# Kernel tuning notes

Hardware: AMD Instinct MI355X
Metric: run time of the kernel (lower is better)

## Reference

```python
import jax, jax.numpy as jnp
import numpy as np

N = 1_000_000          # number of RoIs
C = 4                  # num_class (foreground classes)
IMG_H, IMG_W = 1080.0, 1920.0
BBOX_MEAN = jnp.array([0.0, 0.0, 0.0, 0.0], jnp.float32)
BBOX_STD = jnp.array([0.1, 0.1, 0.2, 0.2], jnp.float32)
THR_OBJ = 0.2          # threshold_objectness
THR_CLS = 0.1          # thresholds[0]
MIN_W, MIN_H = 6.0, 6.0
MAX_CAND = 300         # nms max_candidate_n
OVERLAP = 0.5          # nms overlap_ratio
TOP_N = 100            # nms top_n


def setup_inputs() -> dict:
    key = jax.random.key(0)
    k1, k2, k3, k4, k5 = jax.random.split(key, 5)
    logits = jax.random.normal(k1, (N, C + 1), jnp.float32) * 2.0
    cls_score_softmax = jax.nn.softmax(logits, axis=-1)          # rows sum to 1, like softmax output
    bbox_pred = jax.random.normal(k2, (N, 4 * (C + 1)), jnp.float32) * 0.5
    x1 = jax.random.uniform(k3, (N,), jnp.float32, 0.0, IMG_W * 0.8)
    y1 = jax.random.uniform(k4, (N,), jnp.float32, 0.0, IMG_H * 0.8)
    wh = jax.random.uniform(k5, (N, 2), jnp.float32, 8.0, 200.0)
    rois = jnp.stack([jnp.zeros((N,), jnp.float32), x1, y1, x1 + wh[:, 0], y1 + wh[:, 1]], axis=1)
    im_info = jnp.array([IMG_H, IMG_W], jnp.float32)
    return {"cls_score_softmax": cls_score_softmax, "bbox_pred": bbox_pred, "rois": rois, "im_info": im_info}


def _pairwise_iou(b):
    # torchvision box_iou convention: area = (x2-x1)*(y2-y1), no +1
    lt = jnp.maximum(b[:, None, :2], b[None, :, :2])
    rb = jnp.minimum(b[:, None, 2:], b[None, :, 2:])
    wh = jnp.clip(rb - lt, 0.0)
    inter = wh[..., 0] * wh[..., 1]
    area = (b[:, 2] - b[:, 0]) * (b[:, 3] - b[:, 1])
    return inter / (area[:, None] + area[None, :] - inter)


def _forward(cls_score_softmax, bbox_pred, rois, im_info):
    h_img, w_img = im_info[0], im_info[1]
    # denormalize deltas and decode against rois (bbox_transform_inv_rcnn)
    deltas = (bbox_pred.reshape(-1, 4) * BBOX_STD + BBOX_MEAN).reshape(-1, C + 1, 4)
    bx = rois[:, 1:]
    w = bx[:, 2] - bx[:, 0] + 1.0
    h = bx[:, 3] - bx[:, 1] + 1.0
    cx = bx[:, 0] + 0.5 * (w - 1.0)
    cy = bx[:, 1] + 0.5 * (h - 1.0)
    pcx = deltas[:, :, 0] * w[:, None] + cx[:, None]
    pcy = deltas[:, :, 1] * h[:, None] + cy[:, None]
    pw = jnp.exp(deltas[:, :, 2]) * w[:, None]
    ph = jnp.exp(deltas[:, :, 3]) * h[:, None]
    pred = jnp.stack([pcx - 0.5 * (pw - 1.0), pcy - 0.5 * (ph - 1.0),
                      pcx + 0.5 * (pw - 1.0), pcy + 0.5 * (ph - 1.0)], axis=-1)  # [N, C+1, 4]
    # refine_out_of_map_bbox: clip to image
    pred = jnp.stack([jnp.clip(pred[..., 0], 0.0, w_img - 1.0),
                      jnp.clip(pred[..., 1], 0.0, h_img - 1.0),
                      jnp.clip(pred[..., 2], 0.0, w_img - 1.0),
                      jnp.clip(pred[..., 3], 0.0, h_img - 1.0)], axis=-1)
    # objectness + class-score filters (masked instead of compacted: jit-friendly)
    mask_obj = (1.0 - cls_score_softmax[:, 0]) >= THR_OBJ
    maxes = jnp.max(cls_score_softmax[:, 1:], axis=1)
    argmaxes = jnp.argmax(cls_score_softmax[:, 1:], axis=1) + 1
    mask_cls = maxes > THR_CLS
    # select the box of the argmax class per row
    box = jnp.take_along_axis(pred, argmaxes[:, None, None], axis=1)[:, 0, :]  # [N, 4]
    bw = box[:, 2] - box[:, 0] + 1.0
    bh = box[:, 3] - box[:, 1] + 1.0
    mask_size = (bw >= MIN_W) | (bh >= MIN_H)  # HEIGHT_OR_WIDTH
    valid = mask_obj & mask_cls & mask_size
    # top-k candidates by max class prob (invalid rows pushed below any real score)
    cand_scores = jnp.where(valid, maxes, -1.0)
    top_vals, top_idx = jax.lax.top_k(cand_scores, MAX_CAND)   # sorted descending
    cand_boxes = box[top_idx]                                   # [M, 4]
    cand_probs = cls_score_softmax[top_idx]                     # [M, C+1]
    cand_valid = top_vals > -0.5
    # greedy NMS over the (score-sorted) candidates
    iou = _pairwise_iou(cand_boxes)
    idx = jnp.arange(MAX_CAND)

    def body(i, keep):
        sup = keep[i] & (iou[i] > OVERLAP) & (idx > i)
        return keep & ~sup

    keep = jax.lax.fori_loop(0, MAX_CAND, body, cand_valid)
    # compact kept rows into the first TOP_N slots (drop-row scatter trick)
    order = jnp.cumsum(keep.astype(jnp.int32)) - 1
    slot = jnp.where(keep & (order < TOP_N), order, TOP_N)
    rows = jnp.concatenate([jnp.zeros((MAX_CAND, 1), cand_boxes.dtype), cand_boxes, cand_probs], axis=1)
    out = jnp.zeros((TOP_N + 1, rows.shape[1]), rows.dtype).at[slot].set(rows)[:TOP_N]
    return out  # [TOP_N, 1 + 4 + (C+1)] = [100, 10], zero-padded past the kept count


def reference(cls_score_softmax, bbox_pred, rois, im_info):
    return _forward(cls_score_softmax, bbox_pred, rois, im_info)
```

## Files before the change

### kernel.cpp

```cpp
#include <hip/hip_runtime.h>
#include <math.h>

#define NBINS 4096
#define CAP   4096
#define MAXC  300
#define MAXCP 320
#define TOPN  100

__device__ __forceinline__ int bin_of(float s) {
    int b = (int)(s * (float)NBINS);
    return b > NBINS-1 ? NBINS-1 : b;
}
__device__ __forceinline__ int subbin_of(float s, int tau) {
    float f = s * (float)NBINS - (float)tau;
    int sb = (int)(f * (float)NBINS);
    sb = sb < 0 ? 0 : (sb > NBINS-1 ? NBINS-1 : sb);
    return sb;
}

__device__ __forceinline__ unsigned long long rdlane64(unsigned long long v, int lane) {
    unsigned int lo = (unsigned int)__builtin_amdgcn_readlane((int)(unsigned int)(v & 0xFFFFFFFFull), lane);
    unsigned int hi = (unsigned int)__builtin_amdgcn_readlane((int)(unsigned int)(v >> 32), lane);
    return ((unsigned long long)hi << 32) | (unsigned long long)lo;
}

__device__ __forceinline__ void decode4(float x1, float y1, float x2, float y2,
                                        float4 d4, float Wimg, float Himg,
                                        float& bx1, float& by1, float& bx2, float& by2)
{
    float w  = x2 - x1 + 1.0f;
    float h  = y2 - y1 + 1.0f;
    float cx = x1 + 0.5f*(w - 1.0f);
    float cy = y1 + 0.5f*(h - 1.0f);
    float d0 = d4.x*0.1f, d1 = d4.y*0.1f, d2 = d4.z*0.2f, d3 = d4.w*0.2f;
    float pcx = d0*w + cx;
    float pcy = d1*h + cy;
    float pw  = expf(d2)*w;
    float ph  = expf(d3)*h;
    bx1 = fminf(fmaxf(pcx - 0.5f*(pw-1.0f), 0.0f), Wimg-1.0f);
    by1 = fminf(fmaxf(pcy - 0.5f*(ph-1.0f), 0.0f), Himg-1.0f);
    bx2 = fminf(fmaxf(pcx + 0.5f*(pw-1.0f), 0.0f), Wimg-1.0f);
    by2 = fminf(fmaxf(pcy + 0.5f*(ph-1.0f), 0.0f), Himg-1.0f);
}

__global__ __launch_bounds__(256)
void rcnn_pass1(const float4* __restrict__ cls4, const float4* __restrict__ bbox4,
                const float4* __restrict__ rois4, const float* __restrict__ iminfo,
                float4* __restrict__ scores4,
                unsigned int* __restrict__ hist, unsigned int* __restrict__ hist2,
                unsigned int* __restrict__ counter, int Ng)
{
    if (blockIdx.x == 0) {
        for (int k = threadIdx.x; k < NBINS; k += 256) { hist[k] = 0u; hist2[k] = 0u; }
        if (threadIdx.x == 0) *counter = 0u;
    }

    int g = blockIdx.x * blockDim.x + threadIdx.x;
    if (g >= Ng) return;

    float c[20], q[20];
    #pragma unroll
    for (int v = 0; v < 5; v++) {
        float4 cv = cls4[5*g + v];
        c[4*v] = cv.x; c[4*v+1] = cv.y; c[4*v+2] = cv.z; c[4*v+3] = cv.w;
        float4 rv = rois4[5*g + v];
        q[4*v] = rv.x; q[4*v+1] = rv.y; q[4*v+2] = rv.z; q[4*v+3] = rv.w;
    }
    float Himg = iminfo[0], Wimg = iminfo[1];

    float s[4];
    #pragma unroll
    for (int j = 0; j < 4; j++) {
        float p0 = c[5*j], p1 = c[5*j+1], p2 = c[5*j+2], p3 = c[5*j+3], p4 = c[5*j+4];
        float m = p1; int a = 1;
        if (p2 > m) { m = p2; a = 2; }
        if (p3 > m) { m = p3; a = 3; }
        if (p4 > m) { m = p4; a = 4; }
        float sc = -1.0f;
        if (((1.0f - p0) >= 0.2f) && (m > 0.1f)) {
            float4 d4 = bbox4[20*g + 5*j + a];
            float bx1, by1, bx2, by2;
            decode4(q[5*j+1], q[5*j+2], q[5*j+3], q[5*j+4], d4, Wimg, Himg, bx1, by1, bx2, by2);
            float bw = bx2 - bx1 + 1.0f;
            float bh = by2 - by1 + 1.0f;
            if ((bw >= 6.0f) || (bh >= 6.0f)) sc = m;
        }
        s[j] = sc;
    }
    scores4[g] = make_float4(s[0], s[1], s[2], s[3]);
}

__global__ __launch_bounds__(1024)
void rcnn_hist(const float4* __restrict__ scores4, unsigned int* __restrict__ hist, int Ng)
{
    __shared__ unsigned int lh[NBINS];
    const int t = threadIdx.x;
    for (int k = t; k < NBINS; k += 1024) lh[k] = 0u;
    __syncthreads();
    int stride = gridDim.x * 1024;
    for (int g = blockIdx.x * 1024 + t; g < Ng; g += stride) {
        float4 s4 = scores4[g];
        float ss[4] = { s4.x, s4.y, s4.z, s4.w };
        #pragma unroll
        for (int j = 0; j < 4; j++)
            if (ss[j] > -0.5f) atomicAdd(&lh[bin_of(ss[j])], 1u);
    }
    __syncthreads();
    for (int k = t; k < NBINS; k += 1024) {
        unsigned int v = lh[k];
        if (v) atomicAdd(&hist[k], v);
    }
}

__global__ __launch_bounds__(1024)
void rcnn_pass2(const unsigned int* __restrict__ hist, int* __restrict__ taubin)
{
    __shared__ unsigned int suf[1024];
    __shared__ int g_sh;
    int t = threadIdx.x;
    suf[t] = hist[4*t] + hist[4*t+1] + hist[4*t+2] + hist[4*t+3];
    __syncthreads();
    for (int d = 1; d < 1024; d <<= 1) {
        unsigned int add = (t + d < 1024) ? suf[t + d] : 0u;
        __syncthreads();
        suf[t] += add;
        __syncthreads();
    }
    if (t == 0) g_sh = -1;
    __syncthreads();
    if (suf[t] >= MAXC && (t == 1023 || suf[t+1] < MAXC)) g_sh = t;
    __syncthreads();
    if (t == 0) {
        int g = g_sh;
        int tau = 0;
        if (g >= 0) {
            unsigned int cum = (g == 1023) ? 0u : suf[g+1];
            tau = 4*g;
            for (int k = 3; k >= 0; k--) {
                cum += hist[4*g + k];
                if (cum >= MAXC) { tau = 4*g + k; break; }
            }
        }
        *taubin = tau;
    }
}

__global__ __launch_bounds__(1024)
void rcnn_hist2(const float4* __restrict__ scores4, const int* __restrict__ taubin,
                unsigned int* __restrict__ hist2, int Ng)
{
    __shared__ unsigned int lh[NBINS];
    const int t = threadIdx.x;
    const int tau = *taubin;
    for (int k = t; k < NBINS; k += 1024) lh[k] = 0u;
    __syncthreads();
    int stride = gridDim.x * 1024;
    for (int g = blockIdx.x * 1024 + t; g < Ng; g += stride) {
        float4 s4 = scores4[g];
        float ss[4] = { s4.x, s4.y, s4.z, s4.w };
        #pragma unroll
        for (int j = 0; j < 4; j++)
            if (ss[j] > -0.5f && bin_of(ss[j]) == tau)
                atomicAdd(&lh[subbin_of(ss[j], tau)], 1u);
    }
    __syncthreads();
    for (int k = t; k < NBINS; k += 1024) {
        unsigned int v = lh[k];
        if (v) atomicAdd(&hist2[k], v);
    }
}

__global__ __launch_bounds__(1024)
void rcnn_pass2b(const unsigned int* __restrict__ hist, const unsigned int* __restrict__ hist2,
                 const int* __restrict__ taubin, int* __restrict__ tau2out)
{
    __shared__ unsigned int red[1024];
    __shared__ unsigned int suf[1024];
    __shared__ int g_sh;
    __shared__ unsigned int need_sh;
    int t = threadIdx.x;
    int tau = *taubin;
    unsigned int acc = 0;
    for (int k = tau + 1 + t; k < NBINS; k += 1024) acc += hist[k];
    red[t] = acc;
    __syncthreads();
    for (int d = 512; d > 0; d >>= 1) { if (t < d) red[t] += red[t + d]; __syncthreads(); }
    if (t == 0) {
        unsigned int C1 = red[0];
        need_sh = (C1 >= MAXC) ? 1u : (unsigned int)(MAXC - C1);
    }
    __syncthreads();
    unsigned int need = need_sh;
    suf[t] = hist2[4*t] + hist2[4*t+1] + hist2[4*t+2] + hist2[4*t+3];
    __syncthreads();
    for (int d = 1; d < 1024; d <<= 1) {
        unsigned int add = (t + d < 1024) ? suf[t + d] : 0u;
        __syncthreads();
        suf[t] += add;
        __syncthreads();
    }
    if (t == 0) g_sh = -1;
    __syncthreads();
    if (suf[t] >= need && (t == 1023 || suf[t+1] < need)) g_sh = t;
    __syncthreads();
    if (t == 0) {
        int g = g_sh;
        int tau2 = 0;
        if (g >= 0) {
            unsigned int cum = (g == 1023) ? 0u : suf[g+1];
            tau2 = 4*g;
            for (int k = 3; k >= 0; k--) {
                cum += hist2[4*g + k];
                if (cum >= need) { tau2 = 4*g + k; break; }
            }
        }
        *tau2out = tau2;
    }
}

__global__ __launch_bounds__(256)
void rcnn_pass3(const float4* __restrict__ scores4, const int* __restrict__ taubin,
                const int* __restrict__ tau2bin,
                unsigned long long* __restrict__ ckey,
                unsigned int* __restrict__ counter, int Ng)
{
    int g = blockIdx.x * blockDim.x + threadIdx.x;
    if (g >= Ng) return;
    float4 s4 = scores4[g];
    int tau = *taubin, tau2 = *tau2bin;
    float ss[4] = { s4.x, s4.y, s4.z, s4.w };
    #pragma unroll
    for (int j = 0; j < 4; j++) {
        float s = ss[j];
        if (s > -0.5f) {
            int bin = bin_of(s);
            bool sel = (bin > tau) || (bin == tau && subbin_of(s, tau) >= tau2);
            if (sel) {
                unsigned int pos = atomicAdd(counter, 1u);
                if (pos < CAP) {
                    unsigned int idx = (unsigned int)(4*g + j);
                    ckey[pos] = ((unsigned long long)__float_as_uint(s) << 32)
                              | (unsigned long long)(~idx);
                }
            }
        }
    }
}

__global__ __launch_bounds__(1024)
void rcnn_prep(const float* __restrict__ cls, const float* __restrict__ bbox,
               const float* __restrict__ rois, const float* __restrict__ iminfo,
               const unsigned long long* __restrict__ ckey,
               const unsigned int* __restrict__ counter,
               unsigned long long* __restrict__ sup_g,
               float4* __restrict__ bx4_g,
               float* __restrict__ pr_g,
               unsigned long long* __restrict__ maskw_g)
{
    __shared__ unsigned long long skey[CAP];
    __shared__ int    tid_[MAXC];
    __shared__ float4 bx4[MAXCP];
    __shared__ unsigned long long maskw[5];
    const int t  = threadIdx.x;
    const int NT = 1024;
    int M = (int)*counter; if (M > CAP) M = CAP;

    for (int i = t; i < M; i += NT)  skey[i] = ckey[i];
    for (int r = t; r < MAXC; r += NT) tid_[r] = -1;
    for (int r = t; r < MAXCP; r += NT) bx4[r] = make_float4(0.f, 0.f, 0.f, 0.f);
    if (t < 5) maskw[t] = 0ull;
    __syncthreads();

    for (int i = t; i < M; i += NT) {
        unsigned long long ki = skey[i];
        int r = 0;
        for (int j = 0; j < M; j++) r += (skey[j] > ki);
        if (r < MAXC) tid_[r] = (int)(~(unsigned int)ki);
    }
    __syncthreads();

    float Himg = iminfo[0], Wimg = iminfo[1];
    for (int r = t; r < MAXC; r += NT) {
        int i = tid_[r];
        if (i >= 0) {
            pr_g[5*r+0] = cls[5*i];   pr_g[5*r+1] = cls[5*i+1];
            pr_g[5*r+2] = cls[5*i+2]; pr_g[5*r+3] = cls[5*i+3];
            pr_g[5*r+4] = cls[5*i+4];
            float p1 = cls[5*i+1], p2 = cls[5*i+2], p3 = cls[5*i+3], p4 = cls[5*i+4];
            float m = p1; int a = 1;
            if (p2 > m) { m = p2; a = 2; }
            if (p3 > m) { m = p3; a = 3; }
            if (p4 > m) { m = p4; a = 4; }
            float4 d4 = ((const float4*)bbox)[5*i + a];
            float bx1, by1, bx2, by2;
            decode4(rois[5*i+1], rois[5*i+2], rois[5*i+3], rois[5*i+4], d4, Wimg, Himg, bx1, by1, bx2, by2);
            float4 B = make_float4(bx1, by1, bx2, by2);
            bx4[r] = B;
            bx4_g[r] = B;
            atomicOr(&maskw[r>>6], 1ull << (r & 63));
        }
    }
    __syncthreads();

    if (t < 5) maskw_g[t] = maskw[t];

    for (int task = t; task < MAXC*5; task += NT) {
        int w = task / MAXC;
        int i = task - w*MAXC;
        unsigned long long bits = 0ull;
        int j0 = w << 6;
        if (j0 + 63 > i) {
            float4 A = bx4[i];
            float areaA = (A.z - A.x)*(A.w - A.y);
            for (int b = 0; b < 64; b++) {
                float4 B = bx4[j0 + b];
                float lx = fmaxf(A.x, B.x), ly = fmaxf(A.y, B.y);
                float rx = fminf(A.z, B.z), ry = fminf(A.w, B.w);
                float iw = fmaxf(rx - lx, 0.0f), ih = fmaxf(ry - ly, 0.0f);
                float inter = iw * ih;
                float areaB = (B.z - B.x)*(B.w - B.y);
                float iou = inter / (areaA + areaB - inter);
                bits |= (iou > 0.5f) ? (1ull << b) : 0ull;
            }
            unsigned long long jgt = (i < j0) ? ~0ull
                                  : ((i - j0) >= 63 ? 0ull : ~((1ull << (i - j0 + 1)) - 1ull));
            bits &= jgt & maskw[w];
        }
        sup_g[i*5 + w] = bits;
    }
}

__global__ __launch_bounds__(64, 1)
void rcnn_nms(const unsigned long long* __restrict__ sup_g,
              const float4* __restrict__ bx4_g,
              const float* __restrict__ pr_g,
              const unsigned long long* __restrict__ maskw_g,
              float* __restrict__ out)
{
    __shared__ float orows[TOPN*10];
    const int l = threadIdx.x;

    unsigned long long A0 = sup_g[l*5+0], A1 = sup_g[l*5+1], A2 = sup_g[l*5+2],
                       A3 = sup_g[l*5+3], A4 = sup_g[l*5+4];
    unsigned long long B0 = sup_g[(64+l)*5+0], B1 = sup_g[(64+l)*5+1], B2 = sup_g[(64+l)*5+2],
                       B3 = sup_g[(64+l)*5+3], B4 = sup_g[(64+l)*5+4];
    unsigned long long C0 = sup_g[(128+l)*5+0], C1 = sup_g[(128+l)*5+1], C2 = sup_g[(128+l)*5+2],
                       C3 = sup_g[(128+l)*5+3], C4 = sup_g[(128+l)*5+4];
    unsigned long long D0 = sup_g[(192+l)*5+0], D1 = sup_g[(192+l)*5+1], D2 = sup_g[(192+l)*5+2],
                       D3 = sup_g[(192+l)*5+3], D4 = sup_g[(192+l)*5+4];
    bool e = (l < MAXC - 256);
    unsigned long long E0 = e ? sup_g[(256+l)*5+0] : 0ull,
                       E1 = e ? sup_g[(256+l)*5+1] : 0ull,
                       E2 = e ? sup_g[(256+l)*5+2] : 0ull,
                       E3 = e ? sup_g[(256+l)*5+3] : 0ull,
                       E4 = e ? sup_g[(256+l)*5+4] : 0ull;

    unsigned long long kw0 = maskw_g[0], kw1 = maskw_g[1], kw2 = maskw_g[2],
                       kw3 = maskw_g[3], kw4 = maskw_g[4];

#define SCAN_BLK(W0, W1, W2, W3, W4, KWREF, COUNT)                          \
    for (int s2 = 0; s2 < (COUNT); s2++) {                                  \
        unsigned long long m = ((KWREF >> s2) & 1ull) ? ~0ull : 0ull;       \
        kw0 &= ~(rdlane64(W0, s2) & m);                                     \
        kw1 &= ~(rdlane64(W1, s2) & m);                                     \
        kw2 &= ~(rdlane64(W2, s2) & m);                                     \
        kw3 &= ~(rdlane64(W3, s2) & m);                                     \
        kw4 &= ~(rdlane64(W4, s2) & m);                                     \
    }
    SCAN_BLK(A0, A1, A2, A3, A4, kw0, 64)
    SCAN_BLK(B0, B1, B2, B3, B4, kw1, 64)
    SCAN_BLK(C0, C1, C2, C3, C4, kw2, 64)
    SCAN_BLK(D0, D1, D2, D3, D4, kw3, 64)
    SCAN_BLK(E0, E1, E2, E3, E4, kw4, MAXC - 256)
#undef SCAN_BLK

    for (int k = l; k < TOPN*10; k += 64) orows[k] = 0.0f;
    __syncthreads();

    int p0 = __popcll(kw0), p1 = __popcll(kw1), p2 = __popcll(kw2), p3 = __popcll(kw3);
    unsigned long long lmask = (l == 0) ? 0ull : ((~0ull) >> (64 - l));

#define EMIT_BLK(KW, BASE, PRE)                                             \
    if ((KW >> l) & 1ull) {                                                 \
        int r   = (BASE) + l;                                               \
        int ord = (PRE) + __popcll(KW & lmask);                             \
        if (ord < TOPN) {                                                   \
            float4 B = bx4_g[r];                                            \
            float* row = &orows[ord*10];                                    \
            row[0] = 0.0f;                                                  \
            row[1] = B.x; row[2] = B.y; row[3] = B.z; row[4] = B.w;         \
            row[5] = pr_g[5*r+0]; row[6] = pr_g[5*r+1];                     \
            row[7] = pr_g[5*r+2]; row[8] = pr_g[5*r+3];                     \
            row[9] = pr_g[5*r+4];                                           \
        }                                                                   \
    }
    EMIT_BLK(kw0,   0, 0)
    EMIT_BLK(kw1,  64, p0)
    EMIT_BLK(kw2, 128, p0 + p1)
    EMIT_BLK(kw3, 192, p0 + p1 + p2)
    if (l < MAXC - 256) { EMIT_BLK(kw4, 256, p0 + p1 + p2 + p3) }
#undef EMIT_BLK
    __syncthreads();
    for (int k = l; k < TOPN*10; k += 64) out[k] = orows[k];
}

extern "C" void kernel_launch(void* const* d_in, const int* in_sizes, int n_in,
                              void* d_out, int out_size, void* d_ws, size_t ws_size,
                              hipStream_t stream)
{
    const float* cls    = (const float*)d_in[0];
    const float* bbox   = (const float*)d_in[1];
    const float* rois   = (const float*)d_in[2];
    const float* iminfo = (const float*)d_in[3];
    int N  = in_sizes[0] / 5;
    int Ng = N / 4;

    char* ws = (char*)d_ws;
    float* scores = (float*)ws;
    size_t off = ((size_t)N * 4 + 255) & ~(size_t)255;
    unsigned int* hist    = (unsigned int*)(ws + off); off += NBINS * 4;
    unsigned int* hist2   = (unsigned int*)(ws + off); off += NBINS * 4;
    int*          taubin  = (int*)(ws + off);          off += 256;
    int*          tau2bin = (int*)(ws + off);          off += 256;
    unsigned int* counter = (unsigned int*)(ws + off); off += 256;
    unsigned long long* ckey   = (unsigned long long*)(ws + off); off += CAP * 8;
    unsigned long long* sup_g  = (unsigned long long*)(ws + off); off += MAXC * 5 * 8 + 64;
    float4*             bx4_g  = (float4*)(ws + off);             off += MAXC * 16 + 64;
    float*              pr_g   = (float*)(ws + off);              off += MAXC * 5 * 4 + 64;
    unsigned long long* maskw_g= (unsigned long long*)(ws + off); off += 64;

    int blocksG = (Ng + 255) / 256;
    rcnn_pass1<<<blocksG, 256, 0, stream>>>((const float4*)cls, (const float4*)bbox,
                                            (const float4*)rois, iminfo,
                                            (float4*)scores, hist, hist2, counter, Ng);
    rcnn_hist<<<64, 1024, 0, stream>>>((const float4*)scores, hist, Ng);
    rcnn_pass2<<<1, 1024, 0, stream>>>(hist, taubin);
    rcnn_hist2<<<64, 1024, 0, stream>>>((const float4*)scores, taubin, hist2, Ng);
    rcnn_pass2b<<<1, 1024, 0, stream>>>(hist, hist2, taubin, tau2bin);
    rcnn_pass3<<<blocksG, 256, 0, stream>>>((const float4*)scores, taubin, tau2bin,
                                            ckey, counter, Ng);
    rcnn_prep<<<1, 1024, 0, stream>>>(cls, bbox, rois, iminfo, ckey, counter,
                                      sup_g, bx4_g, pr_g, maskw_g);
    rcnn_nms<<<1, 64, 0, stream>>>(sup_g, bx4_g, pr_g, maskw_g, (float*)d_out);
}
```

Before: 229.2 us.

## Fuse scoring with histogram and replace two-level threshold with single fine histogram

Scoring now builds a per-block LDS histogram in the same kernel, which removes a separate pass over the scores. The two-level 4096-bin histogram and its sub-bin refinement give way to a single 16384-bin histogram. Per-block partial histograms are reduced with no global atomics, and the last-arriving block computes the threshold bin, which cuts the launch count from eight to five. The prep kernel's IoU mask build now uses wave ballots instead of per-thread 64-iteration loops. In exchange, the coarser threshold may admit more candidates into compaction and the O(M²) rank sort, and a candidate count above CAP could truncate results.

```diff
diff --git a/kernel.cpp b/kernel.cpp
--- a/kernel.cpp
+++ b/kernel.cpp
@@ -1,21 +1,16 @@
 #include <hip/hip_runtime.h>
 #include <math.h>
 
-#define NBINS 4096
+#define NB1   16384
+#define NPART 256
 #define CAP   4096
 #define MAXC  300
 #define MAXCP 320
 #define TOPN  100
 
-__device__ __forceinline__ int bin_of(float s) {
-    int b = (int)(s * (float)NBINS);
-    return b > NBINS-1 ? NBINS-1 : b;
-}
-__device__ __forceinline__ int subbin_of(float s, int tau) {
-    float f = s * (float)NBINS - (float)tau;
-    int sb = (int)(f * (float)NBINS);
-    sb = sb < 0 ? 0 : (sb > NBINS-1 ? NBINS-1 : sb);
-    return sb;
+__device__ __forceinline__ int bin16(float s) {
+    int b = (int)(s * (float)NB1);
+    return b > NB1-1 ? NB1-1 : b;
 }
 
 __device__ __forceinline__ unsigned long long rdlane64(unsigned long long v, int lane) {
@@ -43,199 +38,122 @@
     by2 = fminf(fmaxf(pcy + 0.5f*(ph-1.0f), 0.0f), Himg-1.0f);
 }
 
+__global__ __launch_bounds__(512)
+void k1_score_hist(const float4* __restrict__ cls4, const float4* __restrict__ bbox4,
+                   const float4* __restrict__ rois4, const float* __restrict__ iminfo,
+                   float4* __restrict__ scores4, unsigned int* __restrict__ hist_part,
+                   unsigned int* __restrict__ counter, unsigned int* __restrict__ doneflag,
+                   int Ng)
+{
+    __shared__ unsigned int lh[NB1];
+    const int t = threadIdx.x, bid = blockIdx.x;
+    for (int k = t; k < NB1; k += 512) lh[k] = 0u;
+    if (bid == 0 && t == 0) { *counter = 0u; *doneflag = 0u; }
+    __syncthreads();
+
+    float Himg = iminfo[0], Wimg = iminfo[1];
+    int stride = gridDim.x * 512;
+    for (int g = bid*512 + t; g < Ng; g += stride) {
+        float c[20], q[20];
+        #pragma unroll
+        for (int v = 0; v < 5; v++) {
+            float4 cv = cls4[5*g + v];
+            c[4*v] = cv.x; c[4*v+1] = cv.y; c[4*v+2] = cv.z; c[4*v+3] = cv.w;
+            float4 rv = rois4[5*g + v];
+            q[4*v] = rv.x; q[4*v+1] = rv.y; q[4*v+2] = rv.z; q[4*v+3] = rv.w;
+        }
+        float s[4];
+        #pragma unroll
+        for (int j = 0; j < 4; j++) {
+            float p0 = c[5*j], p1 = c[5*j+1], p2 = c[5*j+2], p3 = c[5*j+3], p4 = c[5*j+4];
+            float m = p1; int a = 1;
+            if (p2 > m) { m = p2; a = 2; }
+            if (p3 > m) { m = p3; a = 3; }
+            if (p4 > m) { m = p4; a = 4; }
+            float sc = -1.0f;
+            if (((1.0f - p0) >= 0.2f) && (m > 0.1f)) {
+                float4 d4 = bbox4[20*g + 5*j + a];
+                float bx1, by1, bx2, by2;
+                decode4(q[5*j+1], q[5*j+2], q[5*j+3], q[5*j+4], d4, Wimg, Himg, bx1, by1, bx2, by2);
+                float bw = bx2 - bx1 + 1.0f;
+                float bh = by2 - by1 + 1.0f;
+                if ((bw >= 6.0f) || (bh >= 6.0f)) sc = m;
+            }
+            s[j] = sc;
+        }
+        scores4[g] = make_float4(s[0], s[1], s[2], s[3]);
+        #pragma unroll
+        for (int j = 0; j < 4; j++)
+            if (s[j] > -0.5f) atomicAdd(&lh[bin16(s[j])], 1u);
+    }
+    __syncthreads();
+    for (int k = t; k < NB1; k += 512) hist_part[bid*NB1 + k] = lh[k];
+}
+
+__global__ __launch_bounds__(512)
+void k2_reduce_tau(const unsigned int* __restrict__ hist_part, unsigned int* __restrict__ hist,
+                   int* __restrict__ taubin, unsigned int* __restrict__ doneflag)
+{
+    const int t = threadIdx.x;
+    const int g = blockIdx.x * 512 + t;
+    unsigned int acc = 0;
+    for (int b = 0; b < NPART; b++) acc += hist_part[b*NB1 + g];
+    hist[g] = acc;
+    __threadfence();
+    __shared__ unsigned int amlast;
+    __shared__ unsigned int suf[512];
+    __shared__ int g_sh;
+    __syncthreads();
+    if (t == 0) amlast = (atomicAdd(doneflag, 1u) == gridDim.x - 1) ? 1u : 0u;
+    __syncthreads();
+    if (!amlast) return;
+    __threadfence();
+
+    unsigned int ssum = 0;
+    int base = t * 32;
+    for (int k = 0; k < 32; k++) ssum += hist[base + k];
+    suf[t] = ssum;
+    __syncthreads();
+    for (int d = 1; d < 512; d <<= 1) {
+        unsigned int add = (t + d < 512) ? suf[t + d] : 0u;
+        __syncthreads();
+        suf[t] += add;
+        __syncthreads();
+    }
+    if (t == 0) g_sh = -1;
+    __syncthreads();
+    if (suf[t] >= MAXC && (t == 511 || suf[t+1] < MAXC)) g_sh = t;
+    __syncthreads();
+    if (t == 0) {
+        int g2 = g_sh;
+        int tau = 0;
+        if (g2 >= 0) {
+            unsigned int cum = (g2 == 511) ? 0u : suf[g2+1];
+            tau = 32*g2;
+            for (int k = 31; k >= 0; k--) {
+                cum += hist[32*g2 + k];
+                if (cum >= MAXC) { tau = 32*g2 + k; break; }
+            }
+        }
+        *taubin = tau;
+    }
+}
+
 __global__ __launch_bounds__(256)
-void rcnn_pass1(const float4* __restrict__ cls4, const float4* __restrict__ bbox4,
-                const float4* __restrict__ rois4, const float* __restrict__ iminfo,
-                float4* __restrict__ scores4,
-                unsigned int* __restrict__ hist, unsigned int* __restrict__ hist2,
-                unsigned int* __restrict__ counter, int Ng)
-{
-    if (blockIdx.x == 0) {
-        for (int k = threadIdx.x; k < NBINS; k += 256) { hist[k] = 0u; hist2[k] = 0u; }
-        if (threadIdx.x == 0) *counter = 0u;
-    }
-
-    int g = blockIdx.x * blockDim.x + threadIdx.x;
-    if (g >= Ng) return;
-
-    float c[20], q[20];
-    #pragma unroll
-    for (int v = 0; v < 5; v++) {
-        float4 cv = cls4[5*g + v];
-        c[4*v] = cv.x; c[4*v+1] = cv.y; c[4*v+2] = cv.z; c[4*v+3] = cv.w;
-        float4 rv = rois4[5*g + v];
-        q[4*v] = rv.x; q[4*v+1] = rv.y; q[4*v+2] = rv.z; q[4*v+3] = rv.w;
-    }
-    float Himg = iminfo[0], Wimg = iminfo[1];
-
-    float s[4];
-    #pragma unroll
-    for (int j = 0; j < 4; j++) {
-        float p0 = c[5*j], p1 = c[5*j+1], p2 = c[5*j+2], p3 = c[5*j+3], p4 = c[5*j+4];
-        float m = p1; int a = 1;
-        if (p2 > m) { m = p2; a = 2; }
-        if (p3 > m) { m = p3; a = 3; }
-        if (p4 > m) { m = p4; a = 4; }
-        float sc = -1.0f;
-        if (((1.0f - p0) >= 0.2f) && (m > 0.1f)) {
-            float4 d4 = bbox4[20*g + 5*j + a];
-            float bx1, by1, bx2, by2;
-            decode4(q[5*j+1], q[5*j+2], q[5*j+3], q[5*j+4], d4, Wimg, Himg, bx1, by1, bx2, by2);
-            float bw = bx2 - bx1 + 1.0f;
-            float bh = by2 - by1 + 1.0f;
-            if ((bw >= 6.0f) || (bh >= 6.0f)) sc = m;
-        }
-        s[j] = sc;
-    }
-    scores4[g] = make_float4(s[0], s[1], s[2], s[3]);
-}
-
-__global__ __launch_bounds__(1024)
-void rcnn_hist(const float4* __restrict__ scores4, unsigned int* __restrict__ hist, int Ng)
-{
-    __shared__ unsigned int lh[NBINS];
-    const int t = threadIdx.x;
-    for (int k = t; k < NBINS; k += 1024) lh[k] = 0u;
-    __syncthreads();
-    int stride = gridDim.x * 1024;
-    for (int g = blockIdx.x * 1024 + t; g < Ng; g += stride) {
+void k3_compact(const float4* __restrict__ scores4, const int* __restrict__ taubin,
+                unsigned long long* __restrict__ ckey, unsigned int* __restrict__ counter,
+                int Ng)
+{
+    int g = blockIdx.x * 256 + threadIdx.x;
+    int stride = gridDim.x * 256;
+    int tau = *taubin;
+    for (; g < Ng; g += stride) {
         float4 s4 = scores4[g];
         float ss[4] = { s4.x, s4.y, s4.z, s4.w };
         #pragma unroll
-        for (int j = 0; j < 4; j++)
-            if (ss[j] > -0.5f) atomicAdd(&lh[bin_of(ss[j])], 1u);
-    }
-    __syncthreads();
-    for (int k = t; k < NBINS; k += 1024) {
-        unsigned int v = lh[k];
-        if (v) atomicAdd(&hist[k], v);
-    }
-}
-
-__global__ __launch_bounds__(1024)
-void rcnn_pass2(const unsigned int* __restrict__ hist, int* __restrict__ taubin)
-{
-    __shared__ unsigned int suf[1024];
-    __shared__ int g_sh;
-    int t = threadIdx.x;
-    suf[t] = hist[4*t] + hist[4*t+1] + hist[4*t+2] + hist[4*t+3];
-    __syncthreads();
-    for (int d = 1; d < 1024; d <<= 1) {
-        unsigned int add = (t + d < 1024) ? suf[t + d] : 0u;
-        __syncthreads();
-        suf[t] += add;
-        __syncthreads();
-    }
-    if (t == 0) g_sh = -1;
-    __syncthreads();
-    if (suf[t] >= MAXC && (t == 1023 || suf[t+1] < MAXC)) g_sh = t;
-    __syncthreads();
-    if (t == 0) {
-        int g = g_sh;
-        int tau = 0;
-        if (g >= 0) {
-            unsigned int cum = (g == 1023) ? 0u : suf[g+1];
-            tau = 4*g;
-            for (int k = 3; k >= 0; k--) {
-                cum += hist[4*g + k];
-                if (cum >= MAXC) { tau = 4*g + k; break; }
-            }
-        }
-        *taubin = tau;
-    }
-}
-
-__global__ __launch_bounds__(1024)
-void rcnn_hist2(const float4* __restrict__ scores4, const int* __restrict__ taubin,
-                unsigned int* __restrict__ hist2, int Ng)
-{
-    __shared__ unsigned int lh[NBINS];
-    const int t = threadIdx.x;
-    const int tau = *taubin;
-    for (int k = t; k < NBINS; k += 1024) lh[k] = 0u;
-    __syncthreads();
-    int stride = gridDim.x * 1024;
-    for (int g = blockIdx.x * 1024 + t; g < Ng; g += stride) {
-        float4 s4 = scores4[g];
-        float ss[4] = { s4.x, s4.y, s4.z, s4.w };
-        #pragma unroll
-        for (int j = 0; j < 4; j++)
-            if (ss[j] > -0.5f && bin_of(ss[j]) == tau)
-                atomicAdd(&lh[subbin_of(ss[j], tau)], 1u);
-    }
-    __syncthreads();
-    for (int k = t; k < NBINS; k += 1024) {
-        unsigned int v = lh[k];
-        if (v) atomicAdd(&hist2[k], v);
-    }
-}
-
-__global__ __launch_bounds__(1024)
-void rcnn_pass2b(const unsigned int* __restrict__ hist, const unsigned int* __restrict__ hist2,
-                 const int* __restrict__ taubin, int* __restrict__ tau2out)
-{
-    __shared__ unsigned int red[1024];
-    __shared__ unsigned int suf[1024];
-    __shared__ int g_sh;
-    __shared__ unsigned int need_sh;
-    int t = threadIdx.x;
-    int tau = *taubin;
-    unsigned int acc = 0;
-    for (int k = tau + 1 + t; k < NBINS; k += 1024) acc += hist[k];
-    red[t] = acc;
-    __syncthreads();
-    for (int d = 512; d > 0; d >>= 1) { if (t < d) red[t] += red[t + d]; __syncthreads(); }
-    if (t == 0) {
-        unsigned int C1 = red[0];
-        need_sh = (C1 >= MAXC) ? 1u : (unsigned int)(MAXC - C1);
-    }
-    __syncthreads();
-    unsigned int need = need_sh;
-    suf[t] = hist2[4*t] + hist2[4*t+1] + hist2[4*t+2] + hist2[4*t+3];
-    __syncthreads();
-    for (int d = 1; d < 1024; d <<= 1) {
-        unsigned int add = (t + d < 1024) ? suf[t + d] : 0u;
-        __syncthreads();
-        suf[t] += add;
-        __syncthreads();
-    }
-    if (t == 0) g_sh = -1;
-    __syncthreads();
-    if (suf[t] >= need && (t == 1023 || suf[t+1] < need)) g_sh = t;
-    __syncthreads();
-    if (t == 0) {
-        int g = g_sh;
-        int tau2 = 0;
-        if (g >= 0) {
-            unsigned int cum = (g == 1023) ? 0u : suf[g+1];
-            tau2 = 4*g;
-            for (int k = 3; k >= 0; k--) {
-                cum += hist2[4*g + k];
-                if (cum >= need) { tau2 = 4*g + k; break; }
-            }
-        }
-        *tau2out = tau2;
-    }
-}
-
-__global__ __launch_bounds__(256)
-void rcnn_pass3(const float4* __restrict__ scores4, const int* __restrict__ taubin,
-                const int* __restrict__ tau2bin,
-                unsigned long long* __restrict__ ckey,
-                unsigned int* __restrict__ counter, int Ng)
-{
-    int g = blockIdx.x * blockDim.x + threadIdx.x;
-    if (g >= Ng) return;
-    float4 s4 = scores4[g];
-    int tau = *taubin, tau2 = *tau2bin;
-    float ss[4] = { s4.x, s4.y, s4.z, s4.w };
-    #pragma unroll
-    for (int j = 0; j < 4; j++) {
-        float s = ss[j];
-        if (s > -0.5f) {
-            int bin = bin_of(s);
-            bool sel = (bin > tau) || (bin == tau && subbin_of(s, tau) >= tau2);
-            if (sel) {
+        for (int j = 0; j < 4; j++) {
+            float s = ss[j];
+            if (s > -0.5f && bin16(s) >= tau) {
                 unsigned int pos = atomicAdd(counter, 1u);
                 if (pos < CAP) {
                     unsigned int idx = (unsigned int)(4*g + j);
@@ -248,30 +166,26 @@
 }
 
 __global__ __launch_bounds__(1024)
-void rcnn_prep(const float* __restrict__ cls, const float* __restrict__ bbox,
-               const float* __restrict__ rois, const float* __restrict__ iminfo,
-               const unsigned long long* __restrict__ ckey,
-               const unsigned int* __restrict__ counter,
-               unsigned long long* __restrict__ sup_g,
-               float4* __restrict__ bx4_g,
-               float* __restrict__ pr_g,
-               unsigned long long* __restrict__ maskw_g)
+void k4_prep(const float* __restrict__ cls, const float* __restrict__ bbox,
+             const float* __restrict__ rois, const float* __restrict__ iminfo,
+             const unsigned long long* __restrict__ ckey, const unsigned int* __restrict__ counter,
+             unsigned long long* __restrict__ sup_g, float4* __restrict__ bx4_g,
+             float* __restrict__ pr_g, unsigned long long* __restrict__ maskw_g)
 {
     __shared__ unsigned long long skey[CAP];
     __shared__ int    tid_[MAXC];
     __shared__ float4 bx4[MAXCP];
     __shared__ unsigned long long maskw[5];
-    const int t  = threadIdx.x;
-    const int NT = 1024;
+    const int t = threadIdx.x;
     int M = (int)*counter; if (M > CAP) M = CAP;
 
-    for (int i = t; i < M; i += NT)  skey[i] = ckey[i];
-    for (int r = t; r < MAXC; r += NT) tid_[r] = -1;
-    for (int r = t; r < MAXCP; r += NT) bx4[r] = make_float4(0.f, 0.f, 0.f, 0.f);
+    for (int i = t; i < M; i += 1024) skey[i] = ckey[i];
+    for (int r = t; r < MAXC; r += 1024) tid_[r] = -1;
+    for (int r = t; r < MAXCP; r += 1024) bx4[r] = make_float4(0.f, 0.f, 0.f, 0.f);
     if (t < 5) maskw[t] = 0ull;
     __syncthreads();
 
-    for (int i = t; i < M; i += NT) {
+    for (int i = t; i < M; i += 1024) {
         unsigned long long ki = skey[i];
         int r = 0;
         for (int j = 0; j < M; j++) r += (skey[j] > ki);
@@ -280,7 +194,7 @@
     __syncthreads();
 
     float Himg = iminfo[0], Wimg = iminfo[1];
-    for (int r = t; r < MAXC; r += NT) {
+    for (int r = t; r < MAXC; r += 1024) {
         int i = tid_[r];
         if (i >= 0) {
             pr_g[5*r+0] = cls[5*i];   pr_g[5*r+1] = cls[5*i+1];
@@ -301,41 +215,50 @@
         }
     }
     __syncthreads();
-
     if (t < 5) maskw_g[t] = maskw[t];
 
-    for (int task = t; task < MAXC*5; task += NT) {
-        int w = task / MAXC;
-        int i = task - w*MAXC;
-        unsigned long long bits = 0ull;
-        int j0 = w << 6;
-        if (j0 + 63 > i) {
-            float4 A = bx4[i];
-            float areaA = (A.z - A.x)*(A.w - A.y);
-            for (int b = 0; b < 64; b++) {
-                float4 B = bx4[j0 + b];
-                float lx = fmaxf(A.x, B.x), ly = fmaxf(A.y, B.y);
-                float rx = fminf(A.z, B.z), ry = fminf(A.w, B.w);
-                float iw = fmaxf(rx - lx, 0.0f), ih = fmaxf(ry - ly, 0.0f);
-                float inter = iw * ih;
-                float areaB = (B.z - B.x)*(B.w - B.y);
-                float iou = inter / (areaA + areaB - inter);
-                bits |= (iou > 0.5f) ? (1ull << b) : 0ull;
-            }
-            unsigned long long jgt = (i < j0) ? ~0ull
-                                  : ((i - j0) >= 63 ? 0ull : ~((1ull << (i - j0 + 1)) - 1ull));
-            bits &= jgt & maskw[w];
-        }
-        sup_g[i*5 + w] = bits;
+    const int wv = t >> 6, lane = t & 63;
+    float4 B0 = bx4[lane], B1 = bx4[64+lane], B2 = bx4[128+lane],
+           B3 = bx4[192+lane], B4 = bx4[256+lane];
+    unsigned long long mw0 = maskw[0], mw1 = maskw[1], mw2 = maskw[2],
+                       mw3 = maskw[3], mw4 = maskw[4];
+    for (int i = wv; i < MAXC; i += 16) {
+        float4 A = bx4[i];
+        float areaA = (A.z - A.x)*(A.w - A.y);
+#define IOU_BITS(Bv, W, MW, DST)                                              \
+        {                                                                     \
+            float lx = fmaxf(A.x, Bv.x), ly = fmaxf(A.y, Bv.y);               \
+            float rx = fminf(A.z, Bv.z), ry = fminf(A.w, Bv.w);               \
+            float iw = fmaxf(rx - lx, 0.0f), ih = fmaxf(ry - ly, 0.0f);       \
+            float inter = iw * ih;                                            \
+            float areaB = (Bv.z - Bv.x)*(Bv.w - Bv.y);                        \
+            float iou = inter / (areaA + areaB - inter);                      \
+            unsigned long long bits = __ballot(iou > 0.5f);                   \
+            int j0 = (W) << 6;                                                \
+            unsigned long long jgt = (i < j0) ? ~0ull                         \
+                : ((i - j0) >= 63 ? 0ull : ~((1ull << (i - j0 + 1)) - 1ull)); \
+            DST = bits & jgt & MW;                                            \
+        }
+        unsigned long long r0, r1, r2, r3, r4;
+        IOU_BITS(B0, 0, mw0, r0)
+        IOU_BITS(B1, 1, mw1, r1)
+        IOU_BITS(B2, 2, mw2, r2)
+        IOU_BITS(B3, 3, mw3, r3)
+        IOU_BITS(B4, 4, mw4, r4)
+#undef IOU_BITS
+        if (lane == 0) {
+            sup_g[i*5+0] = r0; sup_g[i*5+1] = r1; sup_g[i*5+2] = r2;
+            sup_g[i*5+3] = r3; sup_g[i*5+4] = r4;
+        }
     }
 }
 
 __global__ __launch_bounds__(64, 1)
-void rcnn_nms(const unsigned long long* __restrict__ sup_g,
-              const float4* __restrict__ bx4_g,
-              const float* __restrict__ pr_g,
-              const unsigned long long* __restrict__ maskw_g,
-              float* __restrict__ out)
+void k5_nms(const unsigned long long* __restrict__ sup_g,
+            const float4* __restrict__ bx4_g,
+            const float* __restrict__ pr_g,
+            const unsigned long long* __restrict__ maskw_g,
+            float* __restrict__ out)
 {
     __shared__ float orows[TOPN*10];
     const int l = threadIdx.x;
@@ -418,28 +341,23 @@
     char* ws = (char*)d_ws;
     float* scores = (float*)ws;
     size_t off = ((size_t)N * 4 + 255) & ~(size_t)255;
-    unsigned int* hist    = (unsigned int*)(ws + off); off += NBINS * 4;
-    unsigned int* hist2   = (unsigned int*)(ws + off); off += NBINS * 4;
-    int*          taubin  = (int*)(ws + off);          off += 256;
-    int*          tau2bin = (int*)(ws + off);          off += 256;
-    unsigned int* counter = (unsigned int*)(ws + off); off += 256;
+    unsigned int* hist_part = (unsigned int*)(ws + off); off += (size_t)NPART * NB1 * 4;
+    unsigned int* hist      = (unsigned int*)(ws + off); off += NB1 * 4;
+    int*          taubin    = (int*)(ws + off);          off += 256;
+    unsigned int* counter   = (unsigned int*)(ws + off); off += 256;
+    unsigned int* doneflag  = (unsigned int*)(ws + off); off += 256;
     unsigned long long* ckey   = (unsigned long long*)(ws + off); off += CAP * 8;
     unsigned long long* sup_g  = (unsigned long long*)(ws + off); off += MAXC * 5 * 8 + 64;
     float4*             bx4_g  = (float4*)(ws + off);             off += MAXC * 16 + 64;
     float*              pr_g   = (float*)(ws + off);              off += MAXC * 5 * 4 + 64;
     unsigned long long* maskw_g= (unsigned long long*)(ws + off); off += 64;
 
-    int blocksG = (Ng + 255) / 256;
-    rcnn_pass1<<<blocksG, 256, 0, stream>>>((const float4*)cls, (const float4*)bbox,
-                                            (const float4*)rois, iminfo,
-                                            (float4*)scores, hist, hist2, counter, Ng);
-    rcnn_hist<<<64, 1024, 0, stream>>>((const float4*)scores, hist, Ng);
-    rcnn_pass2<<<1, 1024, 0, stream>>>(hist, taubin);
-    rcnn_hist2<<<64, 1024, 0, stream>>>((const float4*)scores, taubin, hist2, Ng);
-    rcnn_pass2b<<<1, 1024, 0, stream>>>(hist, hist2, taubin, tau2bin);
-    rcnn_pass3<<<blocksG, 256, 0, stream>>>((const float4*)scores, taubin, tau2bin,
-                                            ckey, counter, Ng);
-    rcnn_prep<<<1, 1024, 0, stream>>>(cls, bbox, rois, iminfo, ckey, counter,
-                                      sup_g, bx4_g, pr_g, maskw_g);
-    rcnn_nms<<<1, 64, 0, stream>>>(sup_g, bx4_g, pr_g, maskw_g, (float*)d_out);
-}
+    k1_score_hist<<<NPART, 512, 0, stream>>>((const float4*)cls, (const float4*)bbox,
+                                             (const float4*)rois, iminfo,
+                                             (float4*)scores, hist_part, counter, doneflag, Ng);
+    k2_reduce_tau<<<NB1/512, 512, 0, stream>>>(hist_part, hist, taubin, doneflag);
+    k3_compact<<<256, 256, 0, stream>>>((const float4*)scores, taubin, ckey, counter, Ng);
+    k4_prep<<<1, 1024, 0, stream>>>(cls, bbox, rois, iminfo, ckey, counter,
+                                    sup_g, bx4_g, pr_g, maskw_g);
+    k5_nms<<<1, 64, 0, stream>>>(sup_g, bx4_g, pr_g, maskw_g, (float*)d_out);
+}
```

Result: slower. 242.3 us (+5.7%).
